# Performance work log

Measured on AMD Instinct MI355X. Metric: run time of the kernel, lower is better.

The kernel has to match this reference:

```python
import jax, jax.numpy as jnp
import numpy as np

N_NODES = 100000
N_EDGES = 1600000
NFEAT = 128
NHID = 128


def setup_inputs() -> dict:
    key = jax.random.key(0)
    k1, k2, k3, k4 = jax.random.split(key, 4)
    x = jax.random.normal(k1, (N_NODES, NFEAT), dtype=jnp.float32)
    edge_index = jax.random.randint(k2, (2, N_EDGES), 0, N_NODES, dtype=jnp.int64)
    # GCNConv params (glorot-style scale)
    W1 = jax.random.normal(k3, (NFEAT, NHID), dtype=jnp.float32) * (1.0 / np.sqrt(NFEAT))
    b1 = jnp.zeros((NHID,), dtype=jnp.float32)
    return {"x": x, "edge_index": edge_index, "W1": W1, "b1": b1}


def gcn_conv(x, edge_index, W, b):
    # PyG GCNConv: out = D^{-1/2} (A + I) D^{-1/2} (x W) + b
    n = x.shape[0]
    loop = jnp.arange(n, dtype=edge_index.dtype)
    src = jnp.concatenate([edge_index[0], loop])  # message sources
    dst = jnp.concatenate([edge_index[1], loop])  # aggregation targets
    deg = jax.ops.segment_sum(jnp.ones_like(dst, dtype=x.dtype), dst, num_segments=n)
    dinv = jnp.where(deg > 0, jax.lax.rsqrt(deg), 0.0)
    norm = dinv[src] * dinv[dst]  # [E+N]
    h = x @ W  # [N, nhid]
    msg = h[src] * norm[:, None]  # gather + scale, [E+N, nhid]
    out = jax.ops.segment_sum(msg, dst, num_segments=n) + b
    return out


def reference(x, edge_index, W1, b1):
    # forward = gc1(x, edge_index) followed by dropout (identity in eval mode)
    return gcn_conv(x, edge_index, W1, b1)
```

## Files before the change

kernel.cpp:

```cpp
#include <hip/hip_runtime.h>
#include <math.h>


#define N_NODES 100000
#define N_EDGES 1600000
#define NF 128
#define LDW 136

#define BSHIFT 9
#define NBUCK 196
#define CHUNK 4096
#define NCHUNK 392
#define SCAN_TOT (NBUCK * NCHUNK)

typedef short bf16x8 __attribute__((ext_vector_type(8)));
typedef float f32x4  __attribute__((ext_vector_type(4)));
typedef unsigned short u16;
typedef unsigned long long u64;

__device__ inline u16 f2bf(float f) {
    unsigned int u = __float_as_uint(f);
    return (u16)((u + 0x7fffu + ((u >> 16) & 1u)) >> 16);
}

__global__ __launch_bounds__(256) void histA_kernel(const int* __restrict__ ei,
                                                    int* __restrict__ histG) {
    __shared__ int hl[NBUCK];
    const int t = threadIdx.x, c = blockIdx.x;
    for (int b = t; b < NBUCK; b += 256) hl[b] = 0;
    __syncthreads();
    const int e0 = c * CHUNK;
    #pragma unroll 4
    for (int it = 0; it < CHUNK / 256; ++it) {
        int e = e0 + it * 256 + t;
        if (e < N_EDGES) atomicAdd(&hl[ei[N_EDGES + e] >> BSHIFT], 1);
    }
    __syncthreads();
    for (int b = t; b < NBUCK; b += 256) histG[b * NCHUNK + c] = hl[b];
}

__global__ __launch_bounds__(256) void scanS1_kernel(const int* __restrict__ histG,
                                                     int* __restrict__ bsum) {
    __shared__ int lds[4];
    const int t = threadIdx.x, b = blockIdx.x;
    int v = histG[b * NCHUNK + t];
    if (t + 256 < NCHUNK) v += histG[b * NCHUNK + t + 256];
    #pragma unroll
    for (int off = 32; off > 0; off >>= 1) v += __shfl_down(v, off);
    if ((t & 63) == 0) lds[t >> 6] = v;
    __syncthreads();
    if (t == 0) bsum[b] = lds[0] + lds[1] + lds[2] + lds[3];
}

__global__ __launch_bounds__(256) void scanS2_kernel(const int* __restrict__ bsum,
                                                     int* __restrict__ bbase) {
    __shared__ int sb[256];
    const int t = threadIdx.x;
    int v = (t < NBUCK) ? bsum[t] : 0;
    sb[t] = v;
    __syncthreads();
    #pragma unroll
    for (int off = 1; off < 256; off <<= 1) {
        int cur = sb[t];
        int add = (t >= off) ? sb[t - off] : 0;
        __syncthreads();
        sb[t] = cur + add;
        __syncthreads();
    }
    if (t < NBUCK) bbase[t] = sb[t] - v;
    if (t == 0) bbase[NBUCK] = N_EDGES;
}

__global__ __launch_bounds__(256) void scanS3_kernel(int* __restrict__ histG,
                                                     const int* __restrict__ bbase) {
    __shared__ int lpair[256];
    const int t = threadIdx.x, b = blockIdx.x;
    int v0 = 0, v1 = 0;
    if (t < NCHUNK / 2) {
        v0 = histG[b * NCHUNK + 2 * t];
        v1 = histG[b * NCHUNK + 2 * t + 1];
    }
    int ps = v0 + v1;
    lpair[t] = ps;
    __syncthreads();
    #pragma unroll
    for (int off = 1; off < 256; off <<= 1) {
        int cur = lpair[t];
        int add = (t >= off) ? lpair[t - off] : 0;
        __syncthreads();
        lpair[t] = cur + add;
        __syncthreads();
    }
    if (t < NCHUNK / 2) {
        int base = bbase[b] + lpair[t] - ps;
        histG[b * NCHUNK + 2 * t] = base;
        histG[b * NCHUNK + 2 * t + 1] = base + v0;
    }
}

__global__ __launch_bounds__(256) void binB_kernel(const int* __restrict__ ei,
                                                   const int* __restrict__ histG,
                                                   u64* __restrict__ ebuf) {
    __shared__ int lbase[NBUCK];
    __shared__ int lcur[NBUCK];
    const int t = threadIdx.x, c = blockIdx.x;
    for (int b = t; b < NBUCK; b += 256) { lbase[b] = histG[b * NCHUNK + c]; lcur[b] = 0; }
    __syncthreads();
    const int e0 = c * CHUNK;
    #pragma unroll 4
    for (int it = 0; it < CHUNK / 256; ++it) {
        int e = e0 + it * 256 + t;
        if (e < N_EDGES) {
            int s = ei[e];
            int d = ei[N_EDGES + e];
            int b = d >> BSHIFT;
            int r = atomicAdd(&lcur[b], 1);
            ebuf[lbase[b] + r] = ((u64)(unsigned)d << 32) | (unsigned)s;
        }
    }
}

__global__ __launch_bounds__(256) void fill3_kernel(const u64* __restrict__ ebuf,
                                                    const int* __restrict__ bbase,
                                                    int* __restrict__ rowptr,
                                                    float* __restrict__ dinv,
                                                    int* __restrict__ slot) {
    __shared__ int lcnt[1 << BSHIFT];
    __shared__ int lpair[256];
    __shared__ int lcur[1 << BSHIFT];
    const int t = threadIdx.x, b = blockIdx.x;
    const int n0 = b << BSHIFT;
    lcnt[t] = 0; lcnt[t + 256] = 0;
    __syncthreads();
    const int lo = bbase[b], hi = bbase[b + 1];
    for (int e = lo + t; e < hi; e += 256) {
        int d = (int)(ebuf[e] >> 32);
        atomicAdd(&lcnt[d - n0], 1);
    }
    __syncthreads();
    int c0 = lcnt[2 * t], c1 = lcnt[2 * t + 1];
    int ps = c0 + c1;
    lpair[t] = ps;
    __syncthreads();
    #pragma unroll
    for (int off = 1; off < 256; off <<= 1) {
        int v = lpair[t];
        int add = (t >= off) ? lpair[t - off] : 0;
        __syncthreads();
        lpair[t] = v + add;
        __syncthreads();
    }
    const int base = lo + lpair[t] - ps;
    lcur[2 * t] = base;
    lcur[2 * t + 1] = base + c0;
    const int n = n0 + 2 * t;
    if (n < N_NODES)     { rowptr[n] = base;          dinv[n] = rsqrtf((float)c0 + 1.0f); }
    if (n + 1 < N_NODES) { rowptr[n + 1] = base + c0; dinv[n + 1] = rsqrtf((float)c1 + 1.0f); }
    if (b == 0 && t == 0) rowptr[N_NODES] = N_EDGES;
    __syncthreads();
    for (int e = lo + t; e < hi; e += 256) {
        u64 p = ebuf[e];
        int d = (int)(p >> 32);
        int s = (int)(p & 0xffffffffu);
        int pos = atomicAdd(&lcur[d - n0], 1);
        slot[pos] = s;
    }
}

__global__ __launch_bounds__(256) void gemm_mfma(const float* __restrict__ x,
                                                 const float* __restrict__ W,
                                                 const float* __restrict__ dinv,
                                                 signed char* __restrict__ h8,
                                                 float* __restrict__ combo) {
    __shared__ u16 Wt[NF * LDW];
    __shared__ u16 xs[64 * LDW];
    const int t = threadIdx.x;
    const int lane = t & 63;
    const int w = t >> 6;
    const int quad = lane >> 4;
    const int m = lane & 15;

    for (int idx = t; idx < NF * NF; idx += 256) {
        int k = idx >> 7, n = idx & 127;
        Wt[n * LDW + k] = f2bf(W[idx]);
    }

    const int rowbase = blockIdx.x * 64;
    for (int it = 0; it < 8; ++it) {
        int linear = it * 256 + t;
        int row = linear >> 5, colq = linear & 31;
        int grow = rowbase + row;
        float4 v = (grow < N_NODES) ? ((const float4*)x)[grow * 32 + colq]
                                    : make_float4(0.f, 0.f, 0.f, 0.f);
        u16* p = &xs[row * LDW + colq * 4];
        p[0] = f2bf(v.x); p[1] = f2bf(v.y); p[2] = f2bf(v.z); p[3] = f2bf(v.w);
    }
    __syncthreads();

    f32x4 acc[8];
    #pragma unroll
    for (int nt = 0; nt < 8; ++nt) acc[nt] = (f32x4){0.f, 0.f, 0.f, 0.f};

    const int r0 = w * 16;
    #pragma unroll
    for (int kt = 0; kt < 4; ++kt) {
        const int k0 = kt * 32;
        bf16x8 a = *(const bf16x8*)&xs[(r0 + m) * LDW + k0 + quad * 8];
        #pragma unroll
        for (int nt = 0; nt < 8; ++nt) {
            bf16x8 bb = *(const bf16x8*)&Wt[(nt * 16 + m) * LDW + k0 + quad * 8];
            acc[nt] = __builtin_amdgcn_mfma_f32_16x16x32_bf16(a, bb, acc[nt], 0, 0, 0);
        }
    }

    float rmax[4];
    #pragma unroll
    for (int r = 0; r < 4; ++r) {
        float mx = 0.f;
        #pragma unroll
        for (int nt = 0; nt < 8; ++nt) mx = fmaxf(mx, fabsf(acc[nt][r]));
        #pragma unroll
        for (int off = 1; off < 16; off <<= 1) mx = fmaxf(mx, __shfl_xor(mx, off));
        rmax[r] = fmaxf(mx, 1e-20f);
    }

    __syncthreads();
    char* xs8 = (char*)xs;
    #pragma unroll
    for (int r = 0; r < 4; ++r) {
        const float inv = 127.f / rmax[r];
        const int row = r0 + quad * 4 + r;
        #pragma unroll
        for (int nt = 0; nt < 8; ++nt) {
            int q = __float2int_rn(acc[nt][r] * inv);
            xs8[row * 144 + nt * 16 + m] = (char)q;
        }
        if (m == 0) {
            int grow = rowbase + row;
            if (grow < N_NODES) combo[grow] = dinv[grow] * (rmax[r] * (1.f / 127.f));
        }
    }
    __syncthreads();

    for (int it = 0; it < 2; ++it) {
        int linear = it * 256 + t;
        int row = linear >> 3, seg = linear & 7;
        int grow = rowbase + row;
        if (grow < N_NODES) {
            uint4 v = *(const uint4*)&xs8[row * 144 + seg * 16];
            ((uint4*)h8)[grow * 8 + seg] = v;
        }
    }
}

__global__ __launch_bounds__(256) void agg_kernel(const signed char* __restrict__ h8,
                                                  const float* __restrict__ dinv,
                                                  const float* __restrict__ combo,
                                                  const int* __restrict__ rowptr,
                                                  const int* __restrict__ slot,
                                                  const float* __restrict__ b,
                                                  float* __restrict__ out) {
    const int wave = threadIdx.x >> 6;
    const int lane = threadIdx.x & 63;
    const int i = blockIdx.x * 4 + wave;
    if (i >= N_NODES) return;

    const float di = dinv[i];
    const int start = rowptr[i];
    const int m = rowptr[i + 1] - start;

    const u16* h2 = (const u16*)h8;
    float2 acc = ((const float2*)b)[lane];
    {
        u16 uv = h2[i * 64 + lane];
        const float w0 = di * combo[i];
        acc.x = fmaf(w0, (float)(signed char)(uv & 0xff), acc.x);
        acc.y = fmaf(w0, (float)(signed char)(uv >> 8), acc.y);
    }

    for (int base = 0; base < m; base += 64) {
        const int mm = min(m - base, 64);
        int   s_l  = (lane < mm) ? slot[start + base + lane] : 0;
        float cw_l = (lane < mm) ? combo[s_l] : 0.0f;
        const int mu = (mm + 7) & ~7;
        for (int j = 0; j < mu; j += 8) {
            int sj[8]; float wj[8]; u16 u[8];
            #pragma unroll
            for (int q = 0; q < 8; ++q) {
                sj[q] = __shfl(s_l, j + q);
                wj[q] = __shfl(cw_l, j + q) * di;
            }
            #pragma unroll
            for (int q = 0; q < 8; ++q) u[q] = h2[sj[q] * 64 + lane];
            #pragma unroll
            for (int q = 0; q < 8; ++q) {
                acc.x = fmaf(wj[q], (float)(signed char)(u[q] & 0xff), acc.x);
                acc.y = fmaf(wj[q], (float)(signed char)(u[q] >> 8), acc.y);
            }
        }
    }
    ((float2*)out)[i * 64 + lane] = acc;
}

extern "C" void kernel_launch(void* const* d_in, const int* in_sizes, int n_in,
                              void* d_out, int out_size, void* d_ws, size_t ws_size,
                              hipStream_t stream) {
    const float* x  = (const float*)d_in[0];
    const int*   ei = (const int*)d_in[1];
    const float* W  = (const float*)d_in[2];
    const float* b  = (const float*)d_in[3];
    float* out = (float*)d_out;

    signed char* h8 = (signed char*)d_ws;
    float* dinv   = (float*)d_ws + 3300000;
    float* combo  = (float*)d_ws + 3400000;
    int*   rowptr = (int*)d_ws + 3500000;
    int*   bbase  = (int*)d_ws + 3610000;
    int*   bsum   = (int*)d_ws + 3612000;
    int*   histG  = (int*)d_ws + 3620000;
    int*   slot   = (int*)d_ws + 3700000;
    u64*   ebuf   = (u64*)((int*)d_ws + 5400000);

    histA_kernel<<<NCHUNK, 256, 0, stream>>>(ei, histG);
    scanS1_kernel<<<NBUCK, 256, 0, stream>>>(histG, bsum);
    scanS2_kernel<<<1, 256, 0, stream>>>(bsum, bbase);
    scanS3_kernel<<<NBUCK, 256, 0, stream>>>(histG, bbase);
    binB_kernel<<<NCHUNK, 256, 0, stream>>>(ei, histG, ebuf);
    fill3_kernel<<<NBUCK, 256, 0, stream>>>(ebuf, bbase, rowptr, dinv, slot);
    gemm_mfma<<<(N_NODES + 63) / 64, 256, 0, stream>>>(x, W, dinv, h8, combo);
    agg_kernel<<<N_NODES / 4, 256, 0, stream>>>(h8, dinv, combo, rowptr, slot, b, out);
}
```

Measured before the change: 223.7 us.

## Fuse GEMM with edge histogram, pack edge buffer to 32-bit, widen aggregation loads

The GEMM now shares one launch with the destination histogram: extra blocks count edges and atomically accumulate bucket sums, which removes the separate histogram and first scan kernels. The GEMM writes a per-row quantization scale, and fill3 folds it with dinv into combo. The edge buffer packs the local destination and source into 32 bits instead of 64, halving binning traffic. The aggregation kernel splits each wave into two halves that read 4 int8 features per lane and process two neighbors at once, then reduces across halves. The cost is extra global atomics and a memset for the bucket sums.

```diff
diff --git a/kernel.cpp b/kernel.cpp
--- a/kernel.cpp
+++ b/kernel.cpp
@@ -11,45 +11,133 @@
 #define NBUCK 196
 #define CHUNK 4096
 #define NCHUNK 392
-#define SCAN_TOT (NBUCK * NCHUNK)
+#define GEMM_BLOCKS 1563
 
 typedef short bf16x8 __attribute__((ext_vector_type(8)));
 typedef float f32x4  __attribute__((ext_vector_type(4)));
 typedef unsigned short u16;
-typedef unsigned long long u64;
 
 __device__ inline u16 f2bf(float f) {
     unsigned int u = __float_as_uint(f);
     return (u16)((u + 0x7fffu + ((u >> 16) & 1u)) >> 16);
 }
 
-__global__ __launch_bounds__(256) void histA_kernel(const int* __restrict__ ei,
-                                                    int* __restrict__ histG) {
-    __shared__ int hl[NBUCK];
-    const int t = threadIdx.x, c = blockIdx.x;
-    for (int b = t; b < NBUCK; b += 256) hl[b] = 0;
-    __syncthreads();
-    const int e0 = c * CHUNK;
-    #pragma unroll 4
-    for (int it = 0; it < CHUNK / 256; ++it) {
-        int e = e0 + it * 256 + t;
-        if (e < N_EDGES) atomicAdd(&hl[ei[N_EDGES + e] >> BSHIFT], 1);
-    }
-    __syncthreads();
-    for (int b = t; b < NBUCK; b += 256) histG[b * NCHUNK + c] = hl[b];
-}
-
-__global__ __launch_bounds__(256) void scanS1_kernel(const int* __restrict__ histG,
+__device__ inline f32x4 unpack4(unsigned int u) {
+    f32x4 r;
+    r[0] = (float)(signed char)(u & 0xff);
+    r[1] = (float)(signed char)((u >> 8) & 0xff);
+    r[2] = (float)(signed char)((u >> 16) & 0xff);
+    r[3] = (float)(signed char)(u >> 24);
+    return r;
+}
+
+__global__ __launch_bounds__(256) void fused1_kernel(const float* __restrict__ x,
+                                                     const float* __restrict__ W,
+                                                     signed char* __restrict__ h8,
+                                                     float* __restrict__ rscale,
+                                                     const int* __restrict__ ei,
+                                                     int* __restrict__ histG,
                                                      int* __restrict__ bsum) {
-    __shared__ int lds[4];
-    const int t = threadIdx.x, b = blockIdx.x;
-    int v = histG[b * NCHUNK + t];
-    if (t + 256 < NCHUNK) v += histG[b * NCHUNK + t + 256];
-    #pragma unroll
-    for (int off = 32; off > 0; off >>= 1) v += __shfl_down(v, off);
-    if ((t & 63) == 0) lds[t >> 6] = v;
-    __syncthreads();
-    if (t == 0) bsum[b] = lds[0] + lds[1] + lds[2] + lds[3];
+    __shared__ u16 Wt[NF * LDW];
+    __shared__ u16 xs[64 * LDW];
+    const int t = threadIdx.x;
+
+    if (blockIdx.x >= GEMM_BLOCKS) {
+        int* hl = (int*)Wt;
+        const int c = blockIdx.x - GEMM_BLOCKS;
+        for (int b = t; b < NBUCK; b += 256) hl[b] = 0;
+        __syncthreads();
+        const int e0 = c * CHUNK;
+        #pragma unroll 4
+        for (int it = 0; it < CHUNK / 256; ++it) {
+            int e = e0 + it * 256 + t;
+            if (e < N_EDGES) atomicAdd(&hl[ei[N_EDGES + e] >> BSHIFT], 1);
+        }
+        __syncthreads();
+        for (int b = t; b < NBUCK; b += 256) {
+            int v = hl[b];
+            histG[b * NCHUNK + c] = v;
+            if (v) atomicAdd(&bsum[b], v);
+        }
+        return;
+    }
+
+    const int lane = t & 63;
+    const int w = t >> 6;
+    const int quad = lane >> 4;
+    const int m = lane & 15;
+
+    for (int idx = t; idx < NF * NF; idx += 256) {
+        int k = idx >> 7, n = idx & 127;
+        Wt[n * LDW + k] = f2bf(W[idx]);
+    }
+
+    const int rowbase = blockIdx.x * 64;
+    for (int it = 0; it < 8; ++it) {
+        int linear = it * 256 + t;
+        int row = linear >> 5, colq = linear & 31;
+        int grow = rowbase + row;
+        float4 v = (grow < N_NODES) ? ((const float4*)x)[grow * 32 + colq]
+                                    : make_float4(0.f, 0.f, 0.f, 0.f);
+        u16* p = &xs[row * LDW + colq * 4];
+        p[0] = f2bf(v.x); p[1] = f2bf(v.y); p[2] = f2bf(v.z); p[3] = f2bf(v.w);
+    }
+    __syncthreads();
+
+    f32x4 acc[8];
+    #pragma unroll
+    for (int nt = 0; nt < 8; ++nt) acc[nt] = (f32x4){0.f, 0.f, 0.f, 0.f};
+
+    const int r0 = w * 16;
+    #pragma unroll
+    for (int kt = 0; kt < 4; ++kt) {
+        const int k0 = kt * 32;
+        bf16x8 a = *(const bf16x8*)&xs[(r0 + m) * LDW + k0 + quad * 8];
+        #pragma unroll
+        for (int nt = 0; nt < 8; ++nt) {
+            bf16x8 bb = *(const bf16x8*)&Wt[(nt * 16 + m) * LDW + k0 + quad * 8];
+            acc[nt] = __builtin_amdgcn_mfma_f32_16x16x32_bf16(a, bb, acc[nt], 0, 0, 0);
+        }
+    }
+
+    float rmax[4];
+    #pragma unroll
+    for (int r = 0; r < 4; ++r) {
+        float mx = 0.f;
+        #pragma unroll
+        for (int nt = 0; nt < 8; ++nt) mx = fmaxf(mx, fabsf(acc[nt][r]));
+        #pragma unroll
+        for (int off = 1; off < 16; off <<= 1) mx = fmaxf(mx, __shfl_xor(mx, off));
+        rmax[r] = fmaxf(mx, 1e-20f);
+    }
+
+    __syncthreads();
+    char* xs8 = (char*)xs;
+    #pragma unroll
+    for (int r = 0; r < 4; ++r) {
+        const float inv = 127.f / rmax[r];
+        const int row = r0 + quad * 4 + r;
+        #pragma unroll
+        for (int nt = 0; nt < 8; ++nt) {
+            int q = __float2int_rn(acc[nt][r] * inv);
+            xs8[row * 144 + nt * 16 + m] = (char)q;
+        }
+        if (m == 0) {
+            int grow = rowbase + row;
+            if (grow < N_NODES) rscale[grow] = rmax[r] * (1.f / 127.f);
+        }
+    }
+    __syncthreads();
+
+    for (int it = 0; it < 2; ++it) {
+        int linear = it * 256 + t;
+        int row = linear >> 3, seg = linear & 7;
+        int grow = rowbase + row;
+        if (grow < N_NODES) {
+            uint4 v = *(const uint4*)&xs8[row * 144 + seg * 16];
+            ((uint4*)h8)[grow * 8 + seg] = v;
+        }
+    }
 }
 
 __global__ __launch_bounds__(256) void scanS2_kernel(const int* __restrict__ bsum,
@@ -100,7 +188,7 @@
 
 __global__ __launch_bounds__(256) void binB_kernel(const int* __restrict__ ei,
                                                    const int* __restrict__ histG,
-                                                   u64* __restrict__ ebuf) {
+                                                   unsigned int* __restrict__ ebuf) {
     __shared__ int lbase[NBUCK];
     __shared__ int lcur[NBUCK];
     const int t = threadIdx.x, c = blockIdx.x;
@@ -115,15 +203,17 @@
             int d = ei[N_EDGES + e];
             int b = d >> BSHIFT;
             int r = atomicAdd(&lcur[b], 1);
-            ebuf[lbase[b] + r] = ((u64)(unsigned)d << 32) | (unsigned)s;
-        }
-    }
-}
-
-__global__ __launch_bounds__(256) void fill3_kernel(const u64* __restrict__ ebuf,
+            ebuf[lbase[b] + r] = ((unsigned)(d & 511) << 17) | (unsigned)s;
+        }
+    }
+}
+
+__global__ __launch_bounds__(256) void fill3_kernel(const unsigned int* __restrict__ ebuf,
                                                     const int* __restrict__ bbase,
+                                                    const float* __restrict__ rscale,
                                                     int* __restrict__ rowptr,
                                                     float* __restrict__ dinv,
+                                                    float* __restrict__ combo,
                                                     int* __restrict__ slot) {
     __shared__ int lcnt[1 << BSHIFT];
     __shared__ int lpair[256];
@@ -134,8 +224,7 @@
     __syncthreads();
     const int lo = bbase[b], hi = bbase[b + 1];
     for (int e = lo + t; e < hi; e += 256) {
-        int d = (int)(ebuf[e] >> 32);
-        atomicAdd(&lcnt[d - n0], 1);
+        atomicAdd(&lcnt[ebuf[e] >> 17], 1);
     }
     __syncthreads();
     int c0 = lcnt[2 * t], c1 = lcnt[2 * t + 1];
@@ -154,102 +243,20 @@
     lcur[2 * t] = base;
     lcur[2 * t + 1] = base + c0;
     const int n = n0 + 2 * t;
-    if (n < N_NODES)     { rowptr[n] = base;          dinv[n] = rsqrtf((float)c0 + 1.0f); }
-    if (n + 1 < N_NODES) { rowptr[n + 1] = base + c0; dinv[n + 1] = rsqrtf((float)c1 + 1.0f); }
+    if (n < N_NODES) {
+        float dv = rsqrtf((float)c0 + 1.0f);
+        rowptr[n] = base; dinv[n] = dv; combo[n] = dv * rscale[n];
+    }
+    if (n + 1 < N_NODES) {
+        float dv = rsqrtf((float)c1 + 1.0f);
+        rowptr[n + 1] = base + c0; dinv[n + 1] = dv; combo[n + 1] = dv * rscale[n + 1];
+    }
     if (b == 0 && t == 0) rowptr[N_NODES] = N_EDGES;
     __syncthreads();
     for (int e = lo + t; e < hi; e += 256) {
-        u64 p = ebuf[e];
-        int d = (int)(p >> 32);
-        int s = (int)(p & 0xffffffffu);
-        int pos = atomicAdd(&lcur[d - n0], 1);
-        slot[pos] = s;
-    }
-}
-
-__global__ __launch_bounds__(256) void gemm_mfma(const float* __restrict__ x,
-                                                 const float* __restrict__ W,
-                                                 const float* __restrict__ dinv,
-                                                 signed char* __restrict__ h8,
-                                                 float* __restrict__ combo) {
-    __shared__ u16 Wt[NF * LDW];
-    __shared__ u16 xs[64 * LDW];
-    const int t = threadIdx.x;
-    const int lane = t & 63;
-    const int w = t >> 6;
-    const int quad = lane >> 4;
-    const int m = lane & 15;
-
-    for (int idx = t; idx < NF * NF; idx += 256) {
-        int k = idx >> 7, n = idx & 127;
-        Wt[n * LDW + k] = f2bf(W[idx]);
-    }
-
-    const int rowbase = blockIdx.x * 64;
-    for (int it = 0; it < 8; ++it) {
-        int linear = it * 256 + t;
-        int row = linear >> 5, colq = linear & 31;
-        int grow = rowbase + row;
-        float4 v = (grow < N_NODES) ? ((const float4*)x)[grow * 32 + colq]
-                                    : make_float4(0.f, 0.f, 0.f, 0.f);
-        u16* p = &xs[row * LDW + colq * 4];
-        p[0] = f2bf(v.x); p[1] = f2bf(v.y); p[2] = f2bf(v.z); p[3] = f2bf(v.w);
-    }
-    __syncthreads();
-
-    f32x4 acc[8];
-    #pragma unroll
-    for (int nt = 0; nt < 8; ++nt) acc[nt] = (f32x4){0.f, 0.f, 0.f, 0.f};
-
-    const int r0 = w * 16;
-    #pragma unroll
-    for (int kt = 0; kt < 4; ++kt) {
-        const int k0 = kt * 32;
-        bf16x8 a = *(const bf16x8*)&xs[(r0 + m) * LDW + k0 + quad * 8];
-        #pragma unroll
-        for (int nt = 0; nt < 8; ++nt) {
-            bf16x8 bb = *(const bf16x8*)&Wt[(nt * 16 + m) * LDW + k0 + quad * 8];
-            acc[nt] = __builtin_amdgcn_mfma_f32_16x16x32_bf16(a, bb, acc[nt], 0, 0, 0);
-        }
-    }
-
-    float rmax[4];
-    #pragma unroll
-    for (int r = 0; r < 4; ++r) {
-        float mx = 0.f;
-        #pragma unroll
-        for (int nt = 0; nt < 8; ++nt) mx = fmaxf(mx, fabsf(acc[nt][r]));
-        #pragma unroll
-        for (int off = 1; off < 16; off <<= 1) mx = fmaxf(mx, __shfl_xor(mx, off));
-        rmax[r] = fmaxf(mx, 1e-20f);
-    }
-
-    __syncthreads();
-    char* xs8 = (char*)xs;
-    #pragma unroll
-    for (int r = 0; r < 4; ++r) {
-        const float inv = 127.f / rmax[r];
-        const int row = r0 + quad * 4 + r;
-        #pragma unroll
-        for (int nt = 0; nt < 8; ++nt) {
-            int q = __float2int_rn(acc[nt][r] * inv);
-            xs8[row * 144 + nt * 16 + m] = (char)q;
-        }
-        if (m == 0) {
-            int grow = rowbase + row;
-            if (grow < N_NODES) combo[grow] = dinv[grow] * (rmax[r] * (1.f / 127.f));
-        }
-    }
-    __syncthreads();
-
-    for (int it = 0; it < 2; ++it) {
-        int linear = it * 256 + t;
-        int row = linear >> 3, seg = linear & 7;
-        int grow = rowbase + row;
-        if (grow < N_NODES) {
-            uint4 v = *(const uint4*)&xs8[row * 144 + seg * 16];
-            ((uint4*)h8)[grow * 8 + seg] = v;
-        }
+        unsigned int p = ebuf[e];
+        int pos = atomicAdd(&lcur[p >> 17], 1);
+        slot[pos] = (int)(p & 0x1ffff);
     }
 }
 
@@ -268,15 +275,12 @@
     const float di = dinv[i];
     const int start = rowptr[i];
     const int m = rowptr[i + 1] - start;
-
-    const u16* h2 = (const u16*)h8;
-    float2 acc = ((const float2*)b)[lane];
-    {
-        u16 uv = h2[i * 64 + lane];
-        const float w0 = di * combo[i];
-        acc.x = fmaf(w0, (float)(signed char)(uv & 0xff), acc.x);
-        acc.y = fmaf(w0, (float)(signed char)(uv >> 8), acc.y);
-    }
+    const int half = lane >> 5;
+    const int col = lane & 31;
+
+    const unsigned int* h4 = (const unsigned int*)h8;
+    f32x4 acc0 = {0.f, 0.f, 0.f, 0.f};
+    f32x4 acc1 = {0.f, 0.f, 0.f, 0.f};
 
     for (int base = 0; base < m; base += 64) {
         const int mm = min(m - base, 64);
@@ -284,22 +288,34 @@
         float cw_l = (lane < mm) ? combo[s_l] : 0.0f;
         const int mu = (mm + 7) & ~7;
         for (int j = 0; j < mu; j += 8) {
-            int sj[8]; float wj[8]; u16 u[8];
             #pragma unroll
-            for (int q = 0; q < 8; ++q) {
-                sj[q] = __shfl(s_l, j + q);
-                wj[q] = __shfl(cw_l, j + q) * di;
+            for (int q = 0; q < 8; q += 2) {
+                int   sj = __shfl(s_l, j + q + half);
+                float wj = __shfl(cw_l, j + q + half) * di;
+                unsigned int u = h4[sj * 32 + col];
+                f32x4 hv = unpack4(u);
+                if (q & 2) acc1 += hv * wj;
+                else       acc0 += hv * wj;
             }
-            #pragma unroll
-            for (int q = 0; q < 8; ++q) u[q] = h2[sj[q] * 64 + lane];
-            #pragma unroll
-            for (int q = 0; q < 8; ++q) {
-                acc.x = fmaf(wj[q], (float)(signed char)(u[q] & 0xff), acc.x);
-                acc.y = fmaf(wj[q], (float)(signed char)(u[q] >> 8), acc.y);
-            }
-        }
-    }
-    ((float2*)out)[i * 64 + lane] = acc;
+        }
+    }
+
+    f32x4 acc = acc0 + acc1;
+    #pragma unroll
+    for (int c = 0; c < 4; ++c) acc[c] += __shfl_xor(acc[c], 32);
+
+    if (lane < 32) {
+        float4 bb = ((const float4*)b)[col];
+        unsigned int uv = h4[i * 32 + col];
+        f32x4 hv = unpack4(uv);
+        const float w0 = di * combo[i];
+        float4 o;
+        o.x = bb.x + acc[0] + w0 * hv[0];
+        o.y = bb.y + acc[1] + w0 * hv[1];
+        o.z = bb.z + acc[2] + w0 * hv[2];
+        o.w = bb.w + acc[3] + w0 * hv[3];
+        ((float4*)out)[i * 32 + col] = o;
+    }
 }
 
 extern "C" void kernel_launch(void* const* d_in, const int* in_sizes, int n_in,
@@ -312,21 +328,23 @@
     float* out = (float*)d_out;
 
     signed char* h8 = (signed char*)d_ws;
-    float* dinv   = (float*)d_ws + 3300000;
-    float* combo  = (float*)d_ws + 3400000;
-    int*   rowptr = (int*)d_ws + 3500000;
-    int*   bbase  = (int*)d_ws + 3610000;
-    int*   bsum   = (int*)d_ws + 3612000;
-    int*   histG  = (int*)d_ws + 3620000;
-    int*   slot   = (int*)d_ws + 3700000;
-    u64*   ebuf   = (u64*)((int*)d_ws + 5400000);
-
-    histA_kernel<<<NCHUNK, 256, 0, stream>>>(ei, histG);
-    scanS1_kernel<<<NBUCK, 256, 0, stream>>>(histG, bsum);
+    float* rscale = (float*)d_ws + 3300000;
+    float* dinv   = (float*)d_ws + 3400000;
+    float* combo  = (float*)d_ws + 3500000;
+    int*   rowptr = (int*)d_ws + 3600000;
+    int*   bbase  = (int*)d_ws + 3750000;
+    int*   bsum   = (int*)d_ws + 3760000;
+    int*   histG  = (int*)d_ws + 3770000;
+    int*   slot   = (int*)d_ws + 4000000;
+    unsigned int* ebuf = (unsigned int*)d_ws + 5700000;
+
+    hipMemsetAsync(bsum, 0, NBUCK * sizeof(int), stream);
+    fused1_kernel<<<GEMM_BLOCKS + NCHUNK, 256, 0, stream>>>(x, W, h8, rscale,
+                                                            ei, histG, bsum);
     scanS2_kernel<<<1, 256, 0, stream>>>(bsum, bbase);
     scanS3_kernel<<<NBUCK, 256, 0, stream>>>(histG, bbase);
     binB_kernel<<<NCHUNK, 256, 0, stream>>>(ei, histG, ebuf);
-    fill3_kernel<<<NBUCK, 256, 0, stream>>>(ebuf, bbase, rowptr, dinv, slot);
-    gemm_mfma<<<(N_NODES + 63) / 64, 256, 0, stream>>>(x, W, dinv, h8, combo);
+    fill3_kernel<<<NBUCK, 256, 0, stream>>>(ebuf, bbase, rscale, rowptr, dinv,
+                                            combo, slot);
     agg_kernel<<<N_NODES / 4, 256, 0, stream>>>(h8, dinv, combo, rowptr, slot, b, out);
 }
```

Result: faster. 219.3 us (-2.0%).
